# Performance work log

Hardware: AMD Instinct MI355X
Metric: run time of the kernel (lower is better)

The kernel has to match this reference:

```python
import jax, jax.numpy as jnp
import numpy as np

B, ENC, Hh, Ww = 32, 512, 14, 14
ATT, EMB, DEC, VOCAB = 512, 512, 512, 10000
MAXLEN = 64  # decode steps = MAXLEN - 1 = 63


def setup_inputs() -> dict:
    key = jax.random.key(0)
    ks = iter(jax.random.split(key, 40))
    def p(shape, s=0.02):
        return jax.random.normal(next(ks), shape, dtype=jnp.float32) * s
    encoder_out = jax.random.normal(next(ks), (B, ENC, Hh, Ww), dtype=jnp.float32)
    encoded_captions = jax.random.randint(next(ks), (B, MAXLEN), 0, VOCAB)
    lens = jax.random.randint(next(ks), (B,), 2, MAXLEN + 1)
    caption_lengths = jnp.sort(lens)[::-1].at[0].set(MAXLEN)  # sorted desc, max forced
    return {
        'encoder_out': encoder_out,
        'encoded_captions': encoded_captions,
        'caption_lengths': caption_lengths,
        'emb_table': p((VOCAB, EMB)),
        'W_enc_att': p((ENC, ATT)), 'b_enc_att': jnp.zeros((ATT,), jnp.float32),
        'W_dec_att': p((DEC, ATT)), 'b_dec_att': jnp.zeros((ATT,), jnp.float32),
        'W_full_att': p((ATT, 1)), 'b_full_att': jnp.zeros((1,), jnp.float32),
        'W_init_h': p((ENC, DEC)), 'b_init_h': jnp.zeros((DEC,), jnp.float32),
        'W_init_c': p((ENC, DEC)), 'b_init_c': jnp.zeros((DEC,), jnp.float32),
        'W_f_beta': p((DEC, ENC)), 'b_f_beta': jnp.zeros((ENC,), jnp.float32),
        'W_ih': p((EMB + ENC, 4 * DEC)), 'b_ih': jnp.zeros((4 * DEC,), jnp.float32),
        'W_hh': p((DEC, 4 * DEC)), 'b_hh': jnp.zeros((4 * DEC,), jnp.float32),
        'W_fc': p((DEC, VOCAB)), 'b_fc': jnp.zeros((VOCAB,), jnp.float32),
    }


def reference(encoder_out, encoded_captions, caption_lengths, emb_table,
              W_enc_att, b_enc_att, W_dec_att, b_dec_att, W_full_att, b_full_att,
              W_init_h, b_init_h, W_init_c, b_init_c, W_f_beta, b_f_beta,
              W_ih, b_ih, W_hh, b_hh, W_fc, b_fc):
    Bs, C, H, W = encoder_out.shape
    enc = encoder_out.transpose(0, 2, 3, 1).reshape(Bs, H * W, C)   # [B,P,ENC]
    emb = emb_table[encoded_captions]                               # [B,L,EMB]
    mean_enc = enc.mean(axis=1)
    h0 = mean_enc @ W_init_h + b_init_h
    c0 = mean_enc @ W_init_c + b_init_c
    dec_len = caption_lengths - 1                                   # [B]
    T = encoded_captions.shape[1] - 1                               # static 63
    enc_att = enc @ W_enc_att + b_enc_att                           # precomputed [B,P,ATT]
    emb_steps = jnp.swapaxes(emb[:, :T, :], 0, 1)                   # [T,B,EMB]
    ts = jnp.arange(T)

    def step(carry, xs):
        h, c = carry
        e_t, t = xs
        # additive attention: full_att(relu(enc_att(enc) + dec_att(h)))
        dec_a = h @ W_dec_att + b_dec_att                           # [B,ATT]
        score = (jax.nn.relu(enc_att + dec_a[:, None, :]) @ W_full_att)[..., 0] + b_full_att[0]
        alpha = jax.nn.softmax(score, axis=1)                       # [B,P]
        awe = jnp.einsum('bp,bpc->bc', alpha, enc)                  # [B,ENC]
        gate = jax.nn.sigmoid(h @ W_f_beta + b_f_beta)
        x = jnp.concatenate([e_t, gate * awe], axis=1)              # [B,EMB+ENC]
        gates = x @ W_ih + b_ih + h @ W_hh + b_hh                   # torch LSTMCell: i,f,g,o
        i, f, g, o = jnp.split(gates, 4, axis=1)
        c_new = jax.nn.sigmoid(f) * c + jax.nn.sigmoid(i) * jnp.tanh(g)
        h_new = jax.nn.sigmoid(o) * jnp.tanh(c_new)
        mask = (t < dec_len)[:, None]                               # active prefix (sorted lens)
        preds = jnp.where(mask, h_new @ W_fc + b_fc, 0.0)           # dropout in eval = identity
        h = jnp.where(mask, h_new, h)
        c = jnp.where(mask, c_new, c)
        return (h, c), preds

    (_, _), preds = jax.lax.scan(step, (h0, c0), (emb_steps, ts))
    return jnp.swapaxes(preds, 0, 1)                                # [B,T,VOCAB]
```

## Files before the change

kernel.cpp:

```cpp
#include <hip/hip_runtime.h>
#include <cstdint>
#include <cstddef>

typedef _Float16 f16;
typedef _Float16 h2 __attribute__((ext_vector_type(2)));
typedef _Float16 h8 __attribute__((ext_vector_type(8)));
typedef float f4v __attribute__((ext_vector_type(4)));

__device__ __forceinline__ h2 u2h2(unsigned u) { return __builtin_bit_cast(h2, u); }
__device__ __forceinline__ unsigned h22u(h2 v) { return __builtin_bit_cast(unsigned, v); }
__device__ __forceinline__ float2 u2f2(unsigned long long u) { return __builtin_bit_cast(float2, u); }

__device__ __forceinline__ float agent_ld_f(const float* p) {
    return __hip_atomic_load(p, __ATOMIC_RELAXED, __HIP_MEMORY_SCOPE_AGENT);
}
__device__ __forceinline__ void agent_st_f(float* p, float v) {
    __hip_atomic_store(p, v, __ATOMIC_RELAXED, __HIP_MEMORY_SCOPE_AGENT);
}
__device__ __forceinline__ unsigned agent_ld_u(const unsigned* p) {
    return __hip_atomic_load(p, __ATOMIC_RELAXED, __HIP_MEMORY_SCOPE_AGENT);
}
__device__ __forceinline__ void agent_st_u(unsigned* p, unsigned v) {
    __hip_atomic_store(p, v, __ATOMIC_RELAXED, __HIP_MEMORY_SCOPE_AGENT);
}
__device__ __forceinline__ unsigned long long agent_ld_u64(const unsigned long long* p) {
    return __hip_atomic_load(p, __ATOMIC_RELAXED, __HIP_MEMORY_SCOPE_AGENT);
}

__device__ __forceinline__ float fdot2(h2 a, h2 b, float c) {
#if __has_builtin(__builtin_amdgcn_fdot2)
    return __builtin_amdgcn_fdot2(a, b, c, false);
#else
    return c + (float)a.x * (float)b.x + (float)a.y * (float)b.y;
#endif
}
__device__ __forceinline__ float sigf(float x) { return 1.0f / (1.0f + expf(-x)); }

__device__ __forceinline__ void gbar32(unsigned* gflags, unsigned epoch, int local) {
    __syncthreads();
    if (threadIdx.x < 64) {
        if (threadIdx.x == 0) {
            asm volatile("s_waitcnt vmcnt(0)" ::: "memory");
            __hip_atomic_store(&gflags[local], epoch, __ATOMIC_RELAXED, __HIP_MEMORY_SCOPE_AGENT);
        }
        const int l = threadIdx.x & 31;
        bool ok;
        do {
            ok = (__hip_atomic_load(&gflags[l], __ATOMIC_RELAXED,
                                    __HIP_MEMORY_SCOPE_AGENT) >= epoch);
            if (!ok) __builtin_amdgcn_s_sleep(1);
        } while (__ballot(ok) != ~0ull);
        asm volatile("" ::: "memory");
    }
    __syncthreads();
}

__global__ void k_prep_w(const float* W_enc, const float* W_dec, const float* W_fb,
                         const float* b_dec, const float* b_fb,
                         const float* b_ih, const float* b_hh,
                         f16* W_encT, f16* Wdf8, float* b_df, float* b_cat) {
    const int S0 = 512 * 512;
    const int S2 = 512 * 1024;
    const int total = S0 + S2 + 1024 + 2048;
    for (int idx = blockIdx.x * 256 + threadIdx.x; idx < total; idx += gridDim.x * 256) {
        int i = idx;
        if (i < S0) { int n = i >> 9, k = i & 511; W_encT[i] = (f16)W_enc[k * 512 + n]; continue; }
        i -= S0;
        if (i < S2) {
            int k8 = i / 8192, r = i % 8192, col = r >> 3, kr = r & 7;
            int k = k8 * 8 + kr;
            float v = (col < 512) ? W_dec[k * 512 + col] : W_fb[k * 512 + (col - 512)];
            Wdf8[i] = (f16)v;
            continue;
        }
        i -= S2;
        if (i < 1024) { b_df[i] = (i < 512) ? b_dec[i] : b_fb[i - 512]; continue; }
        i -= 1024;
        b_cat[i] = b_ih[i] + b_hh[i];
    }
}

__global__ void k_tr_fc(const float* W_fc, f16* W_fcT) {
    __shared__ float tile[64][65];
    int n0 = blockIdx.x * 64;
    int k0 = blockIdx.y * 64;
    int t = threadIdx.x;
#pragma unroll
    for (int i = 0; i < 16; ++i) {
        int lin = t + i * 256;
        int kl = lin >> 6, nl = lin & 63;
        int n = n0 + nl;
        tile[kl][nl] = (n < 10000) ? W_fc[(long)(k0 + kl) * 10000 + n] : 0.0f;
    }
    __syncthreads();
#pragma unroll
    for (int i = 0; i < 2; ++i) {
        int lin = t + i * 256;
        int r = lin >> 3, cv = lin & 7;
        f16 v[8];
#pragma unroll
        for (int kr = 0; kr < 8; ++kr) v[kr] = (f16)tile[cv * 8 + kr][r];
        *(uint4*)&W_fcT[(long)(n0 + r) * 512 + k0 + cv * 8] = *(uint4*)v;
    }
}

__global__ void k_pack_part(const float* W_ih, const float* W_hh, f16* Wpart8) {
    __shared__ float tile[64][65];
    int k0 = blockIdx.x * 64;
    int n0 = blockIdx.y * 64;
    int t = threadIdx.x;
#pragma unroll
    for (int i = 0; i < 16; ++i) {
        int lin = t + i * 256;
        int kl = lin >> 6, nl = lin & 63;
        int k = k0 + kl;
        float v = (k < 512) ? W_ih[(long)k * 2048 + n0 + nl]
                            : W_hh[(long)(k - 512) * 2048 + n0 + nl];
        tile[kl][nl] = v;
    }
    __syncthreads();
#pragma unroll
    for (int i = 0; i < 2; ++i) {
        int lin = t + i * 256;
        int nl = lin & 63, k8l = lin >> 6;
        f16 v[8];
#pragma unroll
        for (int kr = 0; kr < 8; ++kr) v[kr] = (f16)tile[k8l * 8 + kr][nl];
        *(uint4*)&Wpart8[(long)(k0 / 8 + k8l) * 16384 + (long)(n0 + nl) * 8] = *(uint4*)v;
    }
}

__global__ void k_pack_mid(const float* W_ih, f16* Wmid8) {
    __shared__ float tile[64][65];
    int k0 = blockIdx.x * 64;
    int n0 = blockIdx.y * 64;
    int t = threadIdx.x;
#pragma unroll
    for (int i = 0; i < 16; ++i) {
        int lin = t + i * 256;
        int kl = lin >> 6, nl = lin & 63;
        tile[kl][nl] = W_ih[(long)(512 + k0 + kl) * 2048 + n0 + nl];
    }
    __syncthreads();
#pragma unroll
    for (int i = 0; i < 2; ++i) {
        int lin = t + i * 256;
        int nl = lin & 63, k8l = lin >> 6;
        f16 v[8];
#pragma unroll
        for (int kr = 0; kr < 8; ++kr) v[kr] = (f16)tile[k8l * 8 + kr][nl];
        *(uint4*)&Wmid8[(long)(k0 / 8 + k8l) * 16384 + (long)(n0 + nl) * 8] = *(uint4*)v;
    }
}

__global__ void k_prep_enc(const float* enc_out, f16* enc_t, float* mean_enc) {
    __shared__ float tile[64][197];
    int b = blockIdx.x >> 3, cc = blockIdx.x & 7, c0 = cc * 64;
    int t = threadIdx.x;
    const float* src = enc_out + ((long)b * 512 + c0) * 196;
    for (int i = 0; i < 49; ++i) {
        int lin = t + i * 256;
        int cl = lin / 196, p = lin % 196;
        tile[cl][p] = src[cl * 196 + p];
    }
    __syncthreads();
    if (t < 64) {
        float s = 0.f;
        for (int p = 0; p < 196; ++p) s += tile[t][p];
        mean_enc[b * 512 + c0 + t] = s * (1.0f / 196.0f);
    }
    __syncthreads();
    int cl = t & 63, pg = t >> 6;
    for (int i = 0; i < 49; ++i) {
        int p = pg * 49 + i;
        enc_t[((long)(b * 196 + p)) * 512 + c0 + cl] = (f16)tile[cl][p];
    }
}

__global__ void k_h0c0(const float* mean_enc, const float* W_init_h, const float* b_init_h,
                       const float* W_init_c, const float* b_init_c,
                       float* c, f16* h_h, f16* h_all, unsigned* bar) {
    if (blockIdx.x == 64) {
        int t = threadIdx.x;
        for (int i = t; i < 512; i += 256) bar[i] = 0u;
        for (int i = t; i < 32 * 512; i += 256) h_all[(long)2016 * 512 + i] = (f16)0.0f;
        return;
    }
    __shared__ float ms[512];
    int b = blockIdx.x >> 1, which = blockIdx.x & 1;
    const float* W = which ? W_init_c : W_init_h;
    const float* bb = which ? b_init_c : b_init_h;
    int t = threadIdx.x;
    ms[t] = mean_enc[b * 512 + t];
    ms[t + 256] = mean_enc[b * 512 + t + 256];
    __syncthreads();
    for (int jj = 0; jj < 2; ++jj) {
        int j = t + jj * 256;
        float acc = bb[j];
        for (int k = 0; k < 512; ++k) acc += ms[k] * W[k * 512 + j];
        if (which) c[b * 512 + j] = acc;
        else h_h[b * 512 + j] = (f16)acc;
    }
}

__global__ __launch_bounds__(256, 2) void k_encatt(const f16* A, const f16* Bt,
                                                   const float* bias, f16* Cout) {
    __shared__ __align__(16) f16 As[128 * 32];
    __shared__ __align__(16) f16 Bs[128 * 32];
    int m0 = blockIdx.x * 128, n0 = blockIdx.y * 128;
    int t = threadIdx.x, w = t >> 6, lane = t & 63;
    int wm = (w >> 1) * 64, wn = (w & 1) * 64;
    int lm = lane & 15, lq = lane >> 4;
    f4v acc[4][4];
    for (int mi = 0; mi < 4; ++mi)
        for (int ni = 0; ni < 4; ++ni) acc[mi][ni] = (f4v){0.f, 0.f, 0.f, 0.f};
    for (int kb = 0; kb < 512; kb += 32) {
        for (int i = 0; i < 2; ++i) {
            int li = t + i * 256;
            int row = li >> 2, q = li & 3;
            *(uint4*)&As[row * 32 + q * 8] = *(const uint4*)&A[(long)(m0 + row) * 512 + kb + q * 8];
            *(uint4*)&Bs[row * 32 + q * 8] = *(const uint4*)&Bt[(long)(n0 + row) * 512 + kb + q * 8];
        }
        __syncthreads();
        h8 af[4], bf[4];
        for (int i = 0; i < 4; ++i) {
            af[i] = *(const h8*)&As[(wm + i * 16 + lm) * 32 + lq * 8];
            bf[i] = *(const h8*)&Bs[(wn + i * 16 + lm) * 32 + lq * 8];
        }
        for (int mi = 0; mi < 4; ++mi)
            for (int ni = 0; ni < 4; ++ni)
                acc[mi][ni] = __builtin_amdgcn_mfma_f32_16x16x32_f16(af[mi], bf[ni], acc[mi][ni], 0, 0, 0);
        __syncthreads();
    }
    for (int mi = 0; mi < 4; ++mi)
        for (int ni = 0; ni < 4; ++ni)
            for (int r = 0; r < 4; ++r) {
                int row = m0 + wm + mi * 16 + lq * 4 + r;
                int col = n0 + wn + ni * 16 + lm;
                Cout[(long)row * 512 + col] = (f16)(acc[mi][ni][r] + bias[col]);
            }
}

__global__ __launch_bounds__(256, 2) void k_fc(const f16* A, const f16* Bt, const float* bias,
                                               const int* cl, float* out) {
    __shared__ __align__(16) f16 As[128 * 32];
    __shared__ __align__(16) f16 Bs[128 * 32];
    int m0 = blockIdx.x * 128, n0 = blockIdx.y * 128;
    int t = threadIdx.x, w = t >> 6, lane = t & 63;
    int wm = (w >> 1) * 64, wn = (w & 1) * 64;
    int lm = lane & 15, lq = lane >> 4;

    bool myact = false;
    if (t < 128) {
        int row = m0 + t;
        if (row < 2016) {
            int b = row / 63, tt = row - b * 63;
            myact = tt < (cl[b] - 1);
        }
    }
    int anyact = __syncthreads_or((int)myact);
    if (!anyact) {
        for (int i = 0; i < 64; ++i) {
            int idx = t + i * 256;
            int row = m0 + (idx >> 7), col = n0 + (idx & 127);
            if (row < 2016 && col < 10000) out[(long)row * 10000 + col] = 0.0f;
        }
        return;
    }

    f4v acc[4][4];
    for (int mi = 0; mi < 4; ++mi)
        for (int ni = 0; ni < 4; ++ni) acc[mi][ni] = (f4v){0.f, 0.f, 0.f, 0.f};
    for (int kb = 0; kb < 512; kb += 32) {
        for (int i = 0; i < 2; ++i) {
            int li = t + i * 256;
            int row = li >> 2, q = li & 3;
            *(uint4*)&As[row * 32 + q * 8] = *(const uint4*)&A[(long)(m0 + row) * 512 + kb + q * 8];
            *(uint4*)&Bs[row * 32 + q * 8] = *(const uint4*)&Bt[(long)(n0 + row) * 512 + kb + q * 8];
        }
        __syncthreads();
        h8 af[4], bf[4];
        for (int i = 0; i < 4; ++i) {
            af[i] = *(const h8*)&As[(wm + i * 16 + lm) * 32 + lq * 8];
            bf[i] = *(const h8*)&Bs[(wn + i * 16 + lm) * 32 + lq * 8];
        }
        for (int mi = 0; mi < 4; ++mi)
            for (int ni = 0; ni < 4; ++ni)
                acc[mi][ni] = __builtin_amdgcn_mfma_f32_16x16x32_f16(af[mi], bf[ni], acc[mi][ni], 0, 0, 0);
        __syncthreads();
    }
    for (int mi = 0; mi < 4; ++mi)
        for (int ni = 0; ni < 4; ++ni)
            for (int r = 0; r < 4; ++r) {
                int row = m0 + wm + mi * 16 + lq * 4 + r;
                int col = n0 + wn + ni * 16 + lm;
                if (row < 2016 && col < 10000) {
                    int b = row / 63, tt = row - b * 63;
                    bool act = tt < (cl[b] - 1);
                    out[(long)row * 10000 + col] = act ? (acc[mi][ni][r] + bias[col]) : 0.0f;
                }
            }
}

__global__ __launch_bounds__(512, 2) void k_loop(
    const f16* Wdf8, const float* b_df,
    const f16* Wpart8, const f16* Wmid8, const float* b_cat,
    const f16* enc_att_h, const f16* enc_t,
    const float* W_full, const float* emb, const int* caps, const int* cl,
    float* c, f16* h_h, float* da_gp, float* gp_part, float* pawe, float* psum,
    f16* h_all, unsigned* bar) {
    __shared__ __align__(16) unsigned xcat[4 * 512];
    __shared__ float gred[8 * 4 * 64];
    __shared__ float dfred[512];
    __shared__ float das2[512];
    __shared__ float es[32];
    __shared__ float ps4[4];
    __shared__ __align__(16) unsigned xms[4 * 256];
    __shared__ float g3[8 * 4 * 64];
    __shared__ float gsm[256];

    const int bid = blockIdx.x, t = threadIdx.x;
    const int lane = t & 63, w = t >> 6;
    const int local = bid & 31;
    unsigned* gflags = bar + (bid >> 5) * 32;

    const int bg = bid >> 5, b0 = bg * 4;
    const int cg = bid & 31;
    const int jg = bid & 31;
    const int b2 = b0 + ((bid >> 3) & 3), pg = bid & 7;

    float4 wfa = *(const float4*)(W_full + lane * 8);
    float4 wfb = *(const float4*)(W_full + lane * 8 + 4);
    float bc_g = 0.f, bdf = 0.f;
    if (t < 256) bc_g = b_cat[cg * 64 + (t & 63)];
    else if (t < 384) ;
    if (t < 128) bdf = b_df[cg * 32 + (t & 31)];
    const int nc3 = ((t & 63) >> 4) * 512 + jg * 16 + (t & 15);
    const int myb = b0 + (t >> 3);
    const int mycl = (t < 32) ? cl[myb] : 0;
    const int jp = t & 7;
    const int j0 = jg * 16 + jp * 2;
    const int n1 = cg * 64 + lane;
    const int n3 = (lane >> 4) * 512 + jg * 16 + (lane & 15);
    const int dfcol = cg * 32 + (lane & 31);
    const int ksub = lane >> 5, wb2 = w & 3, kh = w >> 2;

    for (int step = 0; step < 63; ++step) {
        {
#pragma unroll
            for (int i = 0; i < 2; ++i) {
                int idx = t + i * 512;
                int b = idx >> 8, off = idx & 255;
                int tok = caps[(b0 + b) * 64 + step];
                float2 ev = *(const float2*)(emb + (long)tok * 512 + off * 2);
                h2 pe; pe.x = (f16)ev.x; pe.y = (f16)ev.y;
                xcat[b * 512 + off] = h22u(pe);
                xcat[b * 512 + 256 + off] = agent_ld_u((const unsigned*)h_h + (b0 + b) * 256 + off);
            }
            __syncthreads();
            {
                const f16* wp = Wpart8 + (long)n1 * 8;
                float a0 = 0.f, a1 = 0.f, a2 = 0.f, a3 = 0.f;
                for (int kk = 0; kk < 16; ++kk) {
                    int k8 = w * 16 + kk;
                    uint4 wv = *(const uint4*)(wp + (long)k8 * 16384);
                    uint4 x0 = *(const uint4*)&xcat[0 * 512 + k8 * 4];
                    uint4 x1 = *(const uint4*)&xcat[1 * 512 + k8 * 4];
                    uint4 x2 = *(const uint4*)&xcat[2 * 512 + k8 * 4];
                    uint4 x3 = *(const uint4*)&xcat[3 * 512 + k8 * 4];
                    a0 = fdot2(u2h2(x0.x), u2h2(wv.x), a0);
                    a0 = fdot2(u2h2(x0.y), u2h2(wv.y), a0);
                    a0 = fdot2(u2h2(x0.z), u2h2(wv.z), a0);
                    a0 = fdot2(u2h2(x0.w), u2h2(wv.w), a0);
                    a1 = fdot2(u2h2(x1.x), u2h2(wv.x), a1);
                    a1 = fdot2(u2h2(x1.y), u2h2(wv.y), a1);
                    a1 = fdot2(u2h2(x1.z), u2h2(wv.z), a1);
                    a1 = fdot2(u2h2(x1.w), u2h2(wv.w), a1);
                    a2 = fdot2(u2h2(x2.x), u2h2(wv.x), a2);
                    a2 = fdot2(u2h2(x2.y), u2h2(wv.y), a2);
                    a2 = fdot2(u2h2(x2.z), u2h2(wv.z), a2);
                    a2 = fdot2(u2h2(x2.w), u2h2(wv.w), a2);
                    a3 = fdot2(u2h2(x3.x), u2h2(wv.x), a3);
                    a3 = fdot2(u2h2(x3.y), u2h2(wv.y), a3);
                    a3 = fdot2(u2h2(x3.z), u2h2(wv.z), a3);
                    a3 = fdot2(u2h2(x3.w), u2h2(wv.w), a3);
                }
                gred[(w * 4 + 0) * 64 + lane] = a0;
                gred[(w * 4 + 1) * 64 + lane] = a1;
                gred[(w * 4 + 2) * 64 + lane] = a2;
                gred[(w * 4 + 3) * 64 + lane] = a3;
            }
            {
                const f16* wdf = Wdf8 + (long)dfcol * 8;
                const unsigned* hx = &xcat[wb2 * 512 + 256];
                int kbase = kh * 32 + ksub * 16;
                float a = 0.f;
                for (int kk = 0; kk < 16; ++kk) {
                    int k8 = kbase + kk;
                    uint4 wv = *(const uint4*)(wdf + (long)k8 * 8192);
                    uint4 xv = *(const uint4*)&hx[k8 * 4];
                    a = fdot2(u2h2(xv.x), u2h2(wv.x), a);
                    a = fdot2(u2h2(xv.y), u2h2(wv.y), a);
                    a = fdot2(u2h2(xv.z), u2h2(wv.z), a);
                    a = fdot2(u2h2(xv.w), u2h2(wv.w), a);
                }
                dfred[(wb2 * 32 + (lane & 31)) * 4 + kh * 2 + ksub] = a;
            }
            __syncthreads();
            if (t < 256) {
                int b = t >> 6, col = t & 63;
                float v = bc_g;
#pragma unroll
                for (int ww = 0; ww < 8; ++ww) v += gred[(ww * 4 + b) * 64 + col];
                agent_st_f(gp_part + (long)(b0 + b) * 2048 + cg * 64 + col, v);
            }
            if (t < 128) {
                int b = t >> 5, col = t & 31;
                const float* dr = &dfred[(b * 32 + col) * 4];
                float v = dr[0] + dr[1] + dr[2] + dr[3] + bdf;
                agent_st_f(da_gp + (long)(b0 + b) * 1024 + cg * 32 + col, v);
            }
        }
        gbar32(gflags, (unsigned)step * 3u + 1u, local);

        {
            das2[t] = agent_ld_f(da_gp + (long)b2 * 1024 + t);
            __syncthreads();
            float4 dv0 = *(const float4*)&das2[lane * 8];
            float4 dv1 = *(const float4*)&das2[lane * 8 + 4];
            int nr = 196 - pg * 25; nr = nr < 25 ? nr : 25;
#pragma unroll
            for (int i = 0; i < 4; ++i) {
                int r = w + i * 8;
                if (r < nr) {
                    int p = pg * 25 + r;
                    uint4 ev = *(const uint4*)(enc_att_h + ((long)b2 * 196 + p) * 512 + lane * 8);
                    h2 e0 = u2h2(ev.x), e1 = u2h2(ev.y), e2 = u2h2(ev.z), e3 = u2h2(ev.w);
                    float a = 0.f;
                    a += fmaxf((float)e0.x + dv0.x, 0.f) * wfa.x;
                    a += fmaxf((float)e0.y + dv0.y, 0.f) * wfa.y;
                    a += fmaxf((float)e1.x + dv0.z, 0.f) * wfa.z;
                    a += fmaxf((float)e1.y + dv0.w, 0.f) * wfa.w;
                    a += fmaxf((float)e2.x + dv1.x, 0.f) * wfb.x;
                    a += fmaxf((float)e2.y + dv1.y, 0.f) * wfb.y;
                    a += fmaxf((float)e3.x + dv1.z, 0.f) * wfb.z;
                    a += fmaxf((float)e3.y + dv1.w, 0.f) * wfb.w;
                    for (int m = 32; m; m >>= 1) a += __shfl_xor(a, m);
                    if (lane == 0) es[r] = expf(a);
                }
            }
            __syncthreads();
            {
                float acc = 0.f;
                const f16* ep = enc_t + ((long)b2 * 196 + pg * 25) * 512 + t;
                for (int r = 0; r < nr; ++r) acc += es[r] * (float)ep[(long)r * 512];
                agent_st_f(pawe + ((long)b2 * 8 + pg) * 512 + t, acc);
                if (t == 0) {
                    float s = 0.f;
                    for (int r = 0; r < nr; ++r) s += es[r];
                    agent_st_f(psum + b2 * 8 + pg, s);
                }
            }
        }
        gbar32(gflags, (unsigned)step * 3u + 2u, local);

        {
            if (t < 4) {
                float s = 0.f;
#pragma unroll
                for (int pgi = 0; pgi < 8; ++pgi)
                    s += agent_ld_f(psum + (b0 + t) * 8 + pgi);
                ps4[t] = 1.0f / s;
            }
            __syncthreads();
#pragma unroll
            for (int i = 0; i < 2; ++i) {
                int idx = t + i * 512;
                int bb = idx >> 8, cp = idx & 255;
                float sx = 0.f, sy = 0.f;
#pragma unroll
                for (int pgi = 0; pgi < 8; ++pgi) {
                    float2 v = u2f2(agent_ld_u64(
                        (const unsigned long long*)pawe + ((long)(b0 + bb) * 8 + pgi) * 256 + cp));
                    sx += v.x; sy += v.y;
                }
                float inv = ps4[bb];
                float2 fb = u2f2(agent_ld_u64(
                    (const unsigned long long*)da_gp + (long)(b0 + bb) * 512 + 256 + cp));
                h2 pa;
                pa.x = (f16)(sigf(fb.x) * sx * inv);
                pa.y = (f16)(sigf(fb.y) * sy * inv);
                xms[bb * 256 + cp] = h22u(pa);
            }
            __syncthreads();
            {
                const f16* wp = Wmid8 + (long)n3 * 8;
                float a0 = 0.f, a1 = 0.f, a2 = 0.f, a3 = 0.f;
                for (int kk = 0; kk < 8; ++kk) {
                    int k8 = w * 8 + kk;
                    uint4 wv = *(const uint4*)(wp + (long)k8 * 16384);
                    uint4 x0 = *(const uint4*)&xms[0 * 256 + k8 * 4];
                    uint4 x1 = *(const uint4*)&xms[1 * 256 + k8 * 4];
                    uint4 x2 = *(const uint4*)&xms[2 * 256 + k8 * 4];
                    uint4 x3 = *(const uint4*)&xms[3 * 256 + k8 * 4];
                    a0 = fdot2(u2h2(x0.x), u2h2(wv.x), a0);
                    a0 = fdot2(u2h2(x0.y), u2h2(wv.y), a0);
                    a0 = fdot2(u2h2(x0.z), u2h2(wv.z), a0);
                    a0 = fdot2(u2h2(x0.w), u2h2(wv.w), a0);
                    a1 = fdot2(u2h2(x1.x), u2h2(wv.x), a1);
                    a1 = fdot2(u2h2(x1.y), u2h2(wv.y), a1);
                    a1 = fdot2(u2h2(x1.z), u2h2(wv.z), a1);
                    a1 = fdot2(u2h2(x1.w), u2h2(wv.w), a1);
                    a2 = fdot2(u2h2(x2.x), u2h2(wv.x), a2);
                    a2 = fdot2(u2h2(x2.y), u2h2(wv.y), a2);
                    a2 = fdot2(u2h2(x2.z), u2h2(wv.z), a2);
                    a2 = fdot2(u2h2(x2.w), u2h2(wv.w), a2);
                    a3 = fdot2(u2h2(x3.x), u2h2(wv.x), a3);
                    a3 = fdot2(u2h2(x3.y), u2h2(wv.y), a3);
                    a3 = fdot2(u2h2(x3.z), u2h2(wv.z), a3);
                    a3 = fdot2(u2h2(x3.w), u2h2(wv.w), a3);
                }
                g3[(w * 4 + 0) * 64 + lane] = a0;
                g3[(w * 4 + 1) * 64 + lane] = a1;
                g3[(w * 4 + 2) * 64 + lane] = a2;
                g3[(w * 4 + 3) * 64 + lane] = a3;
            }
            __syncthreads();
            if (t < 256) {
                int b = t >> 6, l2 = t & 63;
                float v = agent_ld_f(gp_part + (long)(b0 + b) * 2048 + nc3);
#pragma unroll
                for (int ww = 0; ww < 8; ++ww) v += g3[(ww * 4 + b) * 64 + l2];
                gsm[b * 64 + l2] = v;
            }
            __syncthreads();
            if (t < 32) {
                int bl = t >> 3;
                int l0 = jp * 2, l1 = jp * 2 + 1;
                float gi0 = gsm[bl * 64 + l0],      gi1 = gsm[bl * 64 + l1];
                float gf0 = gsm[bl * 64 + 16 + l0], gf1 = gsm[bl * 64 + 16 + l1];
                float gg0 = gsm[bl * 64 + 32 + l0], gg1 = gsm[bl * 64 + 32 + l1];
                float go0 = gsm[bl * 64 + 48 + l0], go1 = gsm[bl * 64 + 48 + l1];
                float2 cold = *(float2*)(c + (long)myb * 512 + j0);
                float cn0 = sigf(gf0) * cold.x + sigf(gi0) * tanhf(gg0);
                float hn0 = sigf(go0) * tanhf(cn0);
                float cn1 = sigf(gf1) * cold.y + sigf(gi1) * tanhf(gg1);
                float hn1 = sigf(go1) * tanhf(cn1);
                h2 oldh = u2h2(agent_ld_u((const unsigned*)h_h + myb * 256 + (j0 >> 1)));
                bool act = step < (mycl - 1);
                float hv0, hv1, cv0, cv1;
                if (act) { hv0 = hn0; hv1 = hn1; cv0 = cn0; cv1 = cn1; }
                else { hv0 = (float)oldh.x; hv1 = (float)oldh.y; cv0 = cold.x; cv1 = cold.y; }
                float2 cw; cw.x = cv0; cw.y = cv1;
                *(float2*)(c + (long)myb * 512 + j0) = cw;
                h2 hp; hp.x = (f16)hv0; hp.y = (f16)hv1;
                unsigned pv = h22u(hp);
                agent_st_u((unsigned*)h_h + myb * 256 + (j0 >> 1), pv);
                *((unsigned*)h_all + ((long)myb * 63 + step) * 256 + (j0 >> 1)) = pv;
            }
        }
        gbar32(gflags, (unsigned)step * 3u + 3u, local);
    }
}

extern "C" void kernel_launch(void* const* d_in, const int* in_sizes, int n_in,
                              void* d_out, int out_size, void* d_ws, size_t ws_size,
                              hipStream_t stream) {
    const float* encoder_out = (const float*)d_in[0];
    const int* caps = (const int*)d_in[1];
    const int* cl = (const int*)d_in[2];
    const float* emb = (const float*)d_in[3];
    const float* W_enc_att = (const float*)d_in[4];
    const float* b_enc_att = (const float*)d_in[5];
    const float* W_dec_att = (const float*)d_in[6];
    const float* b_dec_att = (const float*)d_in[7];
    const float* W_full_att = (const float*)d_in[8];
    const float* W_init_h = (const float*)d_in[10];
    const float* b_init_h = (const float*)d_in[11];
    const float* W_init_c = (const float*)d_in[12];
    const float* b_init_c = (const float*)d_in[13];
    const float* W_f_beta = (const float*)d_in[14];
    const float* b_f_beta = (const float*)d_in[15];
    const float* W_ih = (const float*)d_in[16];
    const float* b_ih = (const float*)d_in[17];
    const float* W_hh = (const float*)d_in[18];
    const float* b_hh = (const float*)d_in[19];
    const float* W_fc = (const float*)d_in[20];
    const float* b_fc = (const float*)d_in[21];

    char* p = (char*)d_ws;
    auto take = [&](size_t bytes) {
        char* r = p;
        p += (bytes + 255) & ~(size_t)255;
        return r;
    };
    f16* enc_t     = (f16*)take((size_t)32 * 196 * 512 * 2);
    f16* enc_att_h = (f16*)take((size_t)32 * 196 * 512 * 2);
    f16* W_encT    = (f16*)take((size_t)512 * 512 * 2);
    f16* W_fcT     = (f16*)take((size_t)10112 * 512 * 2);
    f16* Wdf8      = (f16*)take((size_t)512 * 1024 * 2);
    f16* Wpart8    = (f16*)take((size_t)1024 * 2048 * 2);
    f16* Wmid8     = (f16*)take((size_t)512 * 2048 * 2);
    f16* h_all     = (f16*)take((size_t)2048 * 512 * 2);
    f16* h_h       = (f16*)take((size_t)32 * 512 * 2);
    float* b_df    = (float*)take(1024 * 4);
    float* b_cat   = (float*)take(2048 * 4);
    float* mean_e  = (float*)take((size_t)32 * 512 * 4);
    float* c_st    = (float*)take((size_t)32 * 512 * 4);
    float* da_gp   = (float*)take((size_t)32 * 1024 * 4);
    float* gp_part = (float*)take((size_t)32 * 2048 * 4);
    float* pawe    = (float*)take((size_t)32 * 8 * 512 * 4);
    float* psum    = (float*)take((size_t)256 * 4);
    unsigned* bar  = (unsigned*)take(2048);

    k_prep_w<<<1024, 256, 0, stream>>>(W_enc_att, W_dec_att, W_f_beta,
                                       b_dec_att, b_f_beta, b_ih, b_hh,
                                       W_encT, Wdf8, b_df, b_cat);
    k_tr_fc<<<dim3(158, 8), 256, 0, stream>>>(W_fc, W_fcT);
    k_pack_part<<<dim3(16, 32), 256, 0, stream>>>(W_ih, W_hh, Wpart8);
    k_pack_mid<<<dim3(8, 32), 256, 0, stream>>>(W_ih, Wmid8);
    k_prep_enc<<<256, 256, 0, stream>>>(encoder_out, enc_t, mean_e);
    k_h0c0<<<65, 256, 0, stream>>>(mean_e, W_init_h, b_init_h, W_init_c, b_init_c,
                                   c_st, h_h, h_all, bar);
    k_encatt<<<dim3(49, 4), 256, 0, stream>>>(enc_t, W_encT, b_enc_att, enc_att_h);
    k_loop<<<256, 512, 0, stream>>>(Wdf8, b_df, Wpart8, Wmid8, b_cat,
                                    enc_att_h, enc_t, W_full_att, emb, caps, cl,
                                    c_st, h_h, da_gp, gp_part, pawe, psum, h_all, bar);
    k_fc<<<dim3(16, 79), 256, 0, stream>>>(h_all, W_fcT, b_fc, cl, (float*)d_out);
}
```

Measured before the change: 1.829 ms.

## Cache per-block encoder slices in LDS, prefetch embedding gate work, trim steps per group

Each block now stages its 25-row slices of enc_att and enc_t into LDS once before the loop, so the per-step attention reads come from LDS instead of global memory. The embedding half of the input-gate matvec for the next step is computed before the barrier (warps 0-3), and the dec-att projection is moved onto the other four warps so the two halves of the work split across the block. The loop also ends at the longest caption in each 4-batch group instead of always running 63 steps, and a gp_part load is hoisted earlier. In exchange, LDS use grows by about 50KB, which may limit occupancy against the launch_bounds(512,2) target, and h_all rows for skipped steps are no longer written.

```diff
diff --git a/kernel.cpp b/kernel.cpp
--- a/kernel.cpp
+++ b/kernel.cpp
@@ -311,13 +311,15 @@
     f16* h_all, unsigned* bar) {
     __shared__ __align__(16) unsigned xcat[4 * 512];
     __shared__ float gred[8 * 4 * 64];
-    __shared__ float dfred[512];
+    __shared__ float dfred[256];
     __shared__ float das2[512];
     __shared__ float es[32];
     __shared__ float ps4[4];
     __shared__ __align__(16) unsigned xms[4 * 256];
     __shared__ float g3[8 * 4 * 64];
     __shared__ float gsm[256];
+    __shared__ __align__(16) f16 ea_s[25 * 512];
+    __shared__ __align__(16) f16 et_s[512 * 26];
 
     const int bid = blockIdx.x, t = threadIdx.x;
     const int lane = t & 63, w = t >> 6;
@@ -328,12 +330,12 @@
     const int cg = bid & 31;
     const int jg = bid & 31;
     const int b2 = b0 + ((bid >> 3) & 3), pg = bid & 7;
+    const int nr = (196 - pg * 25) < 25 ? (196 - pg * 25) : 25;
 
     float4 wfa = *(const float4*)(W_full + lane * 8);
     float4 wfb = *(const float4*)(W_full + lane * 8 + 4);
     float bc_g = 0.f, bdf = 0.f;
     if (t < 256) bc_g = b_cat[cg * 64 + (t & 63)];
-    else if (t < 384) ;
     if (t < 128) bdf = b_df[cg * 32 + (t & 31)];
     const int nc3 = ((t & 63) >> 4) * 512 + jg * 16 + (t & 15);
     const int myb = b0 + (t >> 3);
@@ -342,23 +344,88 @@
     const int j0 = jg * 16 + jp * 2;
     const int n1 = cg * 64 + lane;
     const int n3 = (lane >> 4) * 512 + jg * 16 + (lane & 15);
-    const int dfcol = cg * 32 + (lane & 31);
-    const int ksub = lane >> 5, wb2 = w & 3, kh = w >> 2;
-
-    for (int step = 0; step < 63; ++step) {
+
+    int steps_g;
+    {
+        int c0v = cl[b0], c1v = cl[b0 + 1], c2v = cl[b0 + 2], c3v = cl[b0 + 3];
+        int m01 = c0v > c1v ? c0v : c1v;
+        int m23 = c2v > c3v ? c2v : c3v;
+        steps_g = (m01 > m23 ? m01 : m23) - 1;
+    }
+
+    {
+        int r = t >> 6, cv = t & 63;
+        for (int base = 0; base < 25; base += 8) {
+            int rr = base + r;
+            if (rr < nr) {
+                const long rowoff = ((long)b2 * 196 + pg * 25 + rr) * 512 + cv * 8;
+                uint4 va = *(const uint4*)(enc_att_h + rowoff);
+                *(uint4*)&ea_s[rr * 512 + cv * 8] = va;
+                uint4 vt = *(const uint4*)(enc_t + rowoff);
+                f16 tmp[8]; *(uint4*)tmp = vt;
+#pragma unroll
+                for (int e = 0; e < 8; ++e) et_s[(cv * 8 + e) * 26 + rr] = tmp[e];
+            }
+        }
+    }
+
+    auto prework = [&](int sstep) {
+#pragma unroll
+        for (int i = 0; i < 2; ++i) {
+            int idx = t + i * 512;
+            int b = idx >> 8, off = idx & 255;
+            int tok = caps[(b0 + b) * 64 + sstep];
+            float2 ev = *(const float2*)(emb + (long)tok * 512 + off * 2);
+            h2 pe; pe.x = (f16)ev.x; pe.y = (f16)ev.y;
+            xcat[b * 512 + off] = h22u(pe);
+        }
+        __syncthreads();
+        if (w < 4) {
+            const f16* wp = Wpart8 + (long)n1 * 8;
+            float a0 = 0.f, a1 = 0.f, a2 = 0.f, a3 = 0.f;
+            for (int kk = 0; kk < 16; ++kk) {
+                int k8 = w * 16 + kk;
+                uint4 wv = *(const uint4*)(wp + (long)k8 * 16384);
+                uint4 x0 = *(const uint4*)&xcat[0 * 512 + k8 * 4];
+                uint4 x1 = *(const uint4*)&xcat[1 * 512 + k8 * 4];
+                uint4 x2 = *(const uint4*)&xcat[2 * 512 + k8 * 4];
+                uint4 x3 = *(const uint4*)&xcat[3 * 512 + k8 * 4];
+                a0 = fdot2(u2h2(x0.x), u2h2(wv.x), a0);
+                a0 = fdot2(u2h2(x0.y), u2h2(wv.y), a0);
+                a0 = fdot2(u2h2(x0.z), u2h2(wv.z), a0);
+                a0 = fdot2(u2h2(x0.w), u2h2(wv.w), a0);
+                a1 = fdot2(u2h2(x1.x), u2h2(wv.x), a1);
+                a1 = fdot2(u2h2(x1.y), u2h2(wv.y), a1);
+                a1 = fdot2(u2h2(x1.z), u2h2(wv.z), a1);
+                a1 = fdot2(u2h2(x1.w), u2h2(wv.w), a1);
+                a2 = fdot2(u2h2(x2.x), u2h2(wv.x), a2);
+                a2 = fdot2(u2h2(x2.y), u2h2(wv.y), a2);
+                a2 = fdot2(u2h2(x2.z), u2h2(wv.z), a2);
+                a2 = fdot2(u2h2(x2.w), u2h2(wv.w), a2);
+                a3 = fdot2(u2h2(x3.x), u2h2(wv.x), a3);
+                a3 = fdot2(u2h2(x3.y), u2h2(wv.y), a3);
+                a3 = fdot2(u2h2(x3.z), u2h2(wv.z), a3);
+                a3 = fdot2(u2h2(x3.w), u2h2(wv.w), a3);
+            }
+            gred[(w * 4 + 0) * 64 + lane] = a0;
+            gred[(w * 4 + 1) * 64 + lane] = a1;
+            gred[(w * 4 + 2) * 64 + lane] = a2;
+            gred[(w * 4 + 3) * 64 + lane] = a3;
+        }
+    };
+
+    prework(0);
+
+    for (int step = 0; step < steps_g; ++step) {
         {
 #pragma unroll
             for (int i = 0; i < 2; ++i) {
                 int idx = t + i * 512;
                 int b = idx >> 8, off = idx & 255;
-                int tok = caps[(b0 + b) * 64 + step];
-                float2 ev = *(const float2*)(emb + (long)tok * 512 + off * 2);
-                h2 pe; pe.x = (f16)ev.x; pe.y = (f16)ev.y;
-                xcat[b * 512 + off] = h22u(pe);
                 xcat[b * 512 + 256 + off] = agent_ld_u((const unsigned*)h_h + (b0 + b) * 256 + off);
             }
             __syncthreads();
-            {
+            if (w >= 4) {
                 const f16* wp = Wpart8 + (long)n1 * 8;
                 float a0 = 0.f, a1 = 0.f, a2 = 0.f, a3 = 0.f;
                 for (int kk = 0; kk < 16; ++kk) {
@@ -389,13 +456,13 @@
                 gred[(w * 4 + 1) * 64 + lane] = a1;
                 gred[(w * 4 + 2) * 64 + lane] = a2;
                 gred[(w * 4 + 3) * 64 + lane] = a3;
-            }
-            {
-                const f16* wdf = Wdf8 + (long)dfcol * 8;
-                const unsigned* hx = &xcat[wb2 * 512 + 256];
-                int kbase = kh * 32 + ksub * 16;
+            } else {
+                const int dfc = cg * 32 + (lane & 31);
+                const f16* wdf = Wdf8 + (long)dfc * 8;
+                const unsigned* hx = &xcat[w * 512 + 256];
+                int kbase = (lane >> 5) * 32;
                 float a = 0.f;
-                for (int kk = 0; kk < 16; ++kk) {
+                for (int kk = 0; kk < 32; ++kk) {
                     int k8 = kbase + kk;
                     uint4 wv = *(const uint4*)(wdf + (long)k8 * 8192);
                     uint4 xv = *(const uint4*)&hx[k8 * 4];
@@ -404,7 +471,7 @@
                     a = fdot2(u2h2(xv.z), u2h2(wv.z), a);
                     a = fdot2(u2h2(xv.w), u2h2(wv.w), a);
                 }
-                dfred[(wb2 * 32 + (lane & 31)) * 4 + kh * 2 + ksub] = a;
+                dfred[(w * 32 + (lane & 31)) * 2 + (lane >> 5)] = a;
             }
             __syncthreads();
             if (t < 256) {
@@ -416,8 +483,8 @@
             }
             if (t < 128) {
                 int b = t >> 5, col = t & 31;
-                const float* dr = &dfred[(b * 32 + col) * 4];
-                float v = dr[0] + dr[1] + dr[2] + dr[3] + bdf;
+                const float* dr = &dfred[(b * 32 + col) * 2];
+                float v = dr[0] + dr[1] + bdf;
                 agent_st_f(da_gp + (long)(b0 + b) * 1024 + cg * 32 + col, v);
             }
         }
@@ -428,13 +495,11 @@
             __syncthreads();
             float4 dv0 = *(const float4*)&das2[lane * 8];
             float4 dv1 = *(const float4*)&das2[lane * 8 + 4];
-            int nr = 196 - pg * 25; nr = nr < 25 ? nr : 25;
 #pragma unroll
             for (int i = 0; i < 4; ++i) {
                 int r = w + i * 8;
                 if (r < nr) {
-                    int p = pg * 25 + r;
-                    uint4 ev = *(const uint4*)(enc_att_h + ((long)b2 * 196 + p) * 512 + lane * 8);
+                    uint4 ev = *(const uint4*)&ea_s[r * 512 + lane * 8];
                     h2 e0 = u2h2(ev.x), e1 = u2h2(ev.y), e2 = u2h2(ev.z), e3 = u2h2(ev.w);
                     float a = 0.f;
                     a += fmaxf((float)e0.x + dv0.x, 0.f) * wfa.x;
@@ -452,8 +517,7 @@
             __syncthreads();
             {
                 float acc = 0.f;
-                const f16* ep = enc_t + ((long)b2 * 196 + pg * 25) * 512 + t;
-                for (int r = 0; r < nr; ++r) acc += es[r] * (float)ep[(long)r * 512];
+                for (int r = 0; r < nr; ++r) acc += es[r] * (float)et_s[t * 26 + r];
                 agent_st_f(pawe + ((long)b2 * 8 + pg) * 512 + t, acc);
                 if (t == 0) {
                     float s = 0.f;
@@ -465,6 +529,8 @@
         gbar32(gflags, (unsigned)step * 3u + 2u, local);
 
         {
+            float vpart = 0.f;
+            if (t < 256) vpart = agent_ld_f(gp_part + (long)(b0 + (t >> 6)) * 2048 + nc3);
             if (t < 4) {
                 float s = 0.f;
 #pragma unroll
@@ -528,7 +594,7 @@
             __syncthreads();
             if (t < 256) {
                 int b = t >> 6, l2 = t & 63;
-                float v = agent_ld_f(gp_part + (long)(b0 + b) * 2048 + nc3);
+                float v = vpart;
 #pragma unroll
                 for (int ww = 0; ww < 8; ++ww) v += g3[(ww * 4 + b) * 64 + l2];
                 gsm[b * 64 + l2] = v;
@@ -558,6 +624,7 @@
                 agent_st_u((unsigned*)h_h + myb * 256 + (j0 >> 1), pv);
                 *((unsigned*)h_all + ((long)myb * 63 + step) * 256 + (j0 >> 1)) = pv;
             }
+            prework(step + 1);
         }
         gbar32(gflags, (unsigned)step * 3u + 3u, local);
     }
```

After: 1.915 ms. 4.7% more time.

## Cache encoder tiles in LDS, atomically reduce attention, trim loop to group length

Applied to the files above, without the earlier changes.

Each block now preloads its slice of enc_att and a transposed enc_t tile into shared memory once, so later steps read LDS instead of global memory. Partial attention sums go into one buffer through atomic adds, which replaces the 8-way pawe/psum reduction. The gate partials stay block-local because the column mapping is changed so the same block computes both halves. The step loop is cut to the longest caption in the 4-sample group. The costs are about 38KB more LDS per block (launch bounds drop to one block per CU), float atomics that make the summation order non-deterministic, and a zeroing pass for the accumulators every step.

```diff
diff --git a/kernel.cpp b/kernel.cpp
--- a/kernel.cpp
+++ b/kernel.cpp
@@ -16,6 +16,9 @@
 }
 __device__ __forceinline__ void agent_st_f(float* p, float v) {
     __hip_atomic_store(p, v, __ATOMIC_RELAXED, __HIP_MEMORY_SCOPE_AGENT);
+}
+__device__ __forceinline__ void agent_add_f(float* p, float v) {
+    __hip_atomic_fetch_add(p, v, __ATOMIC_RELAXED, __HIP_MEMORY_SCOPE_AGENT);
 }
 __device__ __forceinline__ unsigned agent_ld_u(const unsigned* p) {
     return __hip_atomic_load(p, __ATOMIC_RELAXED, __HIP_MEMORY_SCOPE_AGENT);
@@ -302,22 +305,25 @@
             }
 }
 
-__global__ __launch_bounds__(512, 2) void k_loop(
+__global__ __launch_bounds__(512, 1) void k_loop(
     const f16* Wdf8, const float* b_df,
     const f16* Wpart8, const f16* Wmid8, const float* b_cat,
     const f16* enc_att_h, const f16* enc_t,
     const float* W_full, const float* emb, const int* caps, const int* cl,
-    float* c, f16* h_h, float* da_gp, float* gp_part, float* pawe, float* psum,
+    float* c, f16* h_h, float* da_gp, float* awe2, float* psum2,
     f16* h_all, unsigned* bar) {
     __shared__ __align__(16) unsigned xcat[4 * 512];
     __shared__ float gred[8 * 4 * 64];
     __shared__ float dfred[512];
+    __shared__ float gp_loc[4 * 64];
     __shared__ float das2[512];
     __shared__ float es[32];
     __shared__ float ps4[4];
     __shared__ __align__(16) unsigned xms[4 * 256];
     __shared__ float g3[8 * 4 * 64];
     __shared__ float gsm[256];
+    __shared__ __align__(16) f16 ea_s[25 * 512];
+    __shared__ __align__(16) f16 et_s[512 * 26];
 
     const int bid = blockIdx.x, t = threadIdx.x;
     const int lane = t & 63, w = t >> 6;
@@ -328,25 +334,54 @@
     const int cg = bid & 31;
     const int jg = bid & 31;
     const int b2 = b0 + ((bid >> 3) & 3), pg = bid & 7;
+    const int nr = (196 - pg * 25) < 25 ? (196 - pg * 25) : 25;
 
     float4 wfa = *(const float4*)(W_full + lane * 8);
     float4 wfb = *(const float4*)(W_full + lane * 8 + 4);
+    const int nc3 = ((t & 63) >> 4) * 512 + jg * 16 + (t & 15);
     float bc_g = 0.f, bdf = 0.f;
-    if (t < 256) bc_g = b_cat[cg * 64 + (t & 63)];
-    else if (t < 384) ;
+    if (t < 256) bc_g = b_cat[nc3];
     if (t < 128) bdf = b_df[cg * 32 + (t & 31)];
-    const int nc3 = ((t & 63) >> 4) * 512 + jg * 16 + (t & 15);
     const int myb = b0 + (t >> 3);
     const int mycl = (t < 32) ? cl[myb] : 0;
     const int jp = t & 7;
     const int j0 = jg * 16 + jp * 2;
-    const int n1 = cg * 64 + lane;
-    const int n3 = (lane >> 4) * 512 + jg * 16 + (lane & 15);
+    const int n1 = (lane >> 4) * 512 + cg * 16 + (lane & 15);
+    const int n3 = n1;
     const int dfcol = cg * 32 + (lane & 31);
     const int ksub = lane >> 5, wb2 = w & 3, kh = w >> 2;
 
-    for (int step = 0; step < 63; ++step) {
+    int steps_g;
+    {
+        int c0v = cl[b0], c1v = cl[b0 + 1], c2v = cl[b0 + 2], c3v = cl[b0 + 3];
+        int m01 = c0v > c1v ? c0v : c1v;
+        int m23 = c2v > c3v ? c2v : c3v;
+        steps_g = (m01 > m23 ? m01 : m23) - 1;
+    }
+
+    {
+        int r = t >> 6, cv = t & 63;
+        for (int base = 0; base < 25; base += 8) {
+            int rr = base + r;
+            if (rr < nr) {
+                const long rowoff = ((long)b2 * 196 + pg * 25 + rr) * 512 + cv * 8;
+                uint4 va = *(const uint4*)(enc_att_h + rowoff);
+                *(uint4*)&ea_s[rr * 512 + cv * 8] = va;
+                uint4 vt = *(const uint4*)(enc_t + rowoff);
+                f16 tmp[8]; *(uint4*)tmp = vt;
+#pragma unroll
+                for (int e = 0; e < 8; ++e) et_s[(cv * 8 + e) * 26 + rr] = tmp[e];
+            }
+        }
+    }
+
+    for (int step = 0; step < steps_g; ++step) {
         {
+            if (t < 64) {
+                int idx = local * 64 + t;
+                agent_st_f(awe2 + (long)(b0 + (idx >> 9)) * 512 + (idx & 511), 0.f);
+            }
+            if (local == 0 && t < 4) agent_st_f(psum2 + b0 + t, 0.f);
 #pragma unroll
             for (int i = 0; i < 2; ++i) {
                 int idx = t + i * 512;
@@ -412,7 +447,7 @@
                 float v = bc_g;
 #pragma unroll
                 for (int ww = 0; ww < 8; ++ww) v += gred[(ww * 4 + b) * 64 + col];
-                agent_st_f(gp_part + (long)(b0 + b) * 2048 + cg * 64 + col, v);
+                gp_loc[b * 64 + col] = v;
             }
             if (t < 128) {
                 int b = t >> 5, col = t & 31;
@@ -428,13 +463,11 @@
             __syncthreads();
             float4 dv0 = *(const float4*)&das2[lane * 8];
             float4 dv1 = *(const float4*)&das2[lane * 8 + 4];
-            int nr = 196 - pg * 25; nr = nr < 25 ? nr : 25;
 #pragma unroll
             for (int i = 0; i < 4; ++i) {
                 int r = w + i * 8;
                 if (r < nr) {
-                    int p = pg * 25 + r;
-                    uint4 ev = *(const uint4*)(enc_att_h + ((long)b2 * 196 + p) * 512 + lane * 8);
+                    uint4 ev = *(const uint4*)&ea_s[r * 512 + lane * 8];
                     h2 e0 = u2h2(ev.x), e1 = u2h2(ev.y), e2 = u2h2(ev.z), e3 = u2h2(ev.w);
                     float a = 0.f;
                     a += fmaxf((float)e0.x + dv0.x, 0.f) * wfa.x;
@@ -452,44 +485,32 @@
             __syncthreads();
             {
                 float acc = 0.f;
-                const f16* ep = enc_t + ((long)b2 * 196 + pg * 25) * 512 + t;
-                for (int r = 0; r < nr; ++r) acc += es[r] * (float)ep[(long)r * 512];
-                agent_st_f(pawe + ((long)b2 * 8 + pg) * 512 + t, acc);
+                for (int r = 0; r < nr; ++r) acc += es[r] * (float)et_s[t * 26 + r];
+                agent_add_f(awe2 + (long)b2 * 512 + t, acc);
                 if (t == 0) {
                     float s = 0.f;
                     for (int r = 0; r < nr; ++r) s += es[r];
-                    agent_st_f(psum + b2 * 8 + pg, s);
+                    agent_add_f(psum2 + b2, s);
                 }
             }
         }
         gbar32(gflags, (unsigned)step * 3u + 2u, local);
 
         {
-            if (t < 4) {
-                float s = 0.f;
-#pragma unroll
-                for (int pgi = 0; pgi < 8; ++pgi)
-                    s += agent_ld_f(psum + (b0 + t) * 8 + pgi);
-                ps4[t] = 1.0f / s;
-            }
+            if (t < 4) ps4[t] = 1.0f / agent_ld_f(psum2 + b0 + t);
             __syncthreads();
 #pragma unroll
             for (int i = 0; i < 2; ++i) {
                 int idx = t + i * 512;
                 int bb = idx >> 8, cp = idx & 255;
-                float sx = 0.f, sy = 0.f;
-#pragma unroll
-                for (int pgi = 0; pgi < 8; ++pgi) {
-                    float2 v = u2f2(agent_ld_u64(
-                        (const unsigned long long*)pawe + ((long)(b0 + bb) * 8 + pgi) * 256 + cp));
-                    sx += v.x; sy += v.y;
-                }
+                float2 aw = u2f2(agent_ld_u64(
+                    (const unsigned long long*)awe2 + (long)(b0 + bb) * 256 + cp));
                 float inv = ps4[bb];
                 float2 fb = u2f2(agent_ld_u64(
                     (const unsigned long long*)da_gp + (long)(b0 + bb) * 512 + 256 + cp));
                 h2 pa;
-                pa.x = (f16)(sigf(fb.x) * sx * inv);
-                pa.y = (f16)(sigf(fb.y) * sy * inv);
+                pa.x = (f16)(sigf(fb.x) * aw.x * inv);
+                pa.y = (f16)(sigf(fb.y) * aw.y * inv);
                 xms[bb * 256 + cp] = h22u(pa);
             }
             __syncthreads();
@@ -528,7 +549,7 @@
             __syncthreads();
             if (t < 256) {
                 int b = t >> 6, l2 = t & 63;
-                float v = agent_ld_f(gp_part + (long)(b0 + b) * 2048 + nc3);
+                float v = gp_loc[b * 64 + l2];
 #pragma unroll
                 for (int ww = 0; ww < 8; ++ww) v += g3[(ww * 4 + b) * 64 + l2];
                 gsm[b * 64 + l2] = v;
@@ -608,9 +629,8 @@
     float* mean_e  = (float*)take((size_t)32 * 512 * 4);
     float* c_st    = (float*)take((size_t)32 * 512 * 4);
     float* da_gp   = (float*)take((size_t)32 * 1024 * 4);
-    float* gp_part = (float*)take((size_t)32 * 2048 * 4);
-    float* pawe    = (float*)take((size_t)32 * 8 * 512 * 4);
-    float* psum    = (float*)take((size_t)256 * 4);
+    float* awe2    = (float*)take((size_t)32 * 512 * 4);
+    float* psum2   = (float*)take((size_t)32 * 4);
     unsigned* bar  = (unsigned*)take(2048);
 
     k_prep_w<<<1024, 256, 0, stream>>>(W_enc_att, W_dec_att, W_f_beta,
@@ -625,6 +645,6 @@
     k_encatt<<<dim3(49, 4), 256, 0, stream>>>(enc_t, W_encT, b_enc_att, enc_att_h);
     k_loop<<<256, 512, 0, stream>>>(Wdf8, b_df, Wpart8, Wmid8, b_cat,
                                     enc_att_h, enc_t, W_full_att, emb, caps, cl,
-                                    c_st, h_h, da_gp, gp_part, pawe, psum, h_all, bar);
+                                    c_st, h_h, da_gp, awe2, psum2, h_all, bar);
     k_fc<<<dim3(16, 79), 256, 0, stream>>>(h_all, W_fcT, b_fc, cl, (float*)d_out);
 }
```

Measured after the change: 1.616 ms. 1.13x faster.
